# Optimization experiments

Hardware: AMD Instinct MI355X
Metric: run time of the kernel (lower is better)

Reference implementation:

```python
import jax, jax.numpy as jnp
import numpy as np

N = 50000        # n_nodes
E = 640000       # n_edges
D = 128          # d_model (in_dim == out_dim)
H = 8            # num_heads
DH = D // H      # head dim = 16
EPS = 1e-5


def _batchnorm(x, g, b):
    # BatchNorm1d, training-mode batch statistics (biased variance)
    mu = jnp.mean(x, axis=0)
    var = jnp.mean((x - mu) ** 2, axis=0)
    return (x - mu) * jax.lax.rsqrt(var + EPS) * g + b


def setup_inputs() -> dict:
    key = jax.random.key(0)
    ks = jax.random.split(key, 16)
    s = 0.05
    h = jax.random.normal(ks[0], (N, D), jnp.float32)
    src = jax.random.randint(ks[1], (E,), 0, N)
    # guarantee every node has >= 1 incoming edge (avoids z == 0)
    dst = jnp.concatenate([jnp.arange(N), jax.random.randint(ks[2], (E - N,), 0, N)])
    return {
        "h": h,
        "src": src,
        "dst": dst,
        "WQ": jax.random.normal(ks[3], (D, D), jnp.float32) * s,
        "WK": jax.random.normal(ks[4], (D, D), jnp.float32) * s,
        "WV": jax.random.normal(ks[5], (D, D), jnp.float32) * s,
        "WO": jax.random.normal(ks[6], (D, D), jnp.float32) * s,
        "bO": jnp.zeros((D,), jnp.float32),
        "W1": jax.random.normal(ks[7], (2 * D, D), jnp.float32) * s,
        "b1": jnp.zeros((2 * D,), jnp.float32),
        "W2": jax.random.normal(ks[8], (D, 2 * D), jnp.float32) * s,
        "b2": jnp.zeros((D,), jnp.float32),
        "bn1_g": jnp.ones((D,), jnp.float32),
        "bn1_b": jnp.zeros((D,), jnp.float32),
        "bn2_g": jnp.ones((D,), jnp.float32),
        "bn2_b": jnp.zeros((D,), jnp.float32),
    }


def reference(h, src, dst, WQ, WK, WV, WO, bO, W1, b1, W2, b2, bn1_g, bn1_b, bn2_g, bn2_b):
    n = h.shape[0]
    # projections -> [N, H, DH]
    Q = (h @ WQ.T).reshape(n, H, DH)
    K = (h @ WK.T).reshape(n, H, DH)
    V = (h @ WV.T).reshape(n, H, DH)
    # per-edge score: sum(K[src] * Q[dst]) -> [E, H]; clamp/exp (scaled_exp)
    score = jnp.sum(K[src] * Q[dst], axis=-1) / np.sqrt(DH)
    score = jnp.exp(jnp.clip(score, -5.0, 5.0))
    # scatter-sum weighted values and normalizers to destination nodes
    wV = jax.ops.segment_sum(V[src] * score[..., None], dst, num_segments=n)  # [N,H,DH]
    z = jax.ops.segment_sum(score, dst, num_segments=n)                       # [N,H]
    attn = (wV / z[..., None]).reshape(n, D)
    # O projection + residual + BN1
    h1 = _batchnorm(h + (attn @ WO.T + bO), bn1_g, bn1_b)
    # FFN + residual + BN2
    f = jax.nn.relu(h1 @ W1.T + b1) @ W2.T + b2
    return _batchnorm(h1 + f, bn2_g, bn2_b)
```

## Files before the change

kernel.cpp:

```cpp
#include <hip/hip_runtime.h>
#include <math.h>


#define ND128 16384
typedef _Float16 f16;
typedef __attribute__((ext_vector_type(8))) _Float16 h8;
typedef __attribute__((ext_vector_type(4))) _Float16 h4;
typedef __attribute__((ext_vector_type(2))) _Float16 h2;
typedef __attribute__((ext_vector_type(4))) float f4;
typedef __attribute__((ext_vector_type(2))) float ff2;

__device__ __forceinline__ ff2 fp8x2_dec(unsigned v) {
#if __has_builtin(__builtin_amdgcn_cvt_pk_f32_fp8)
    return __builtin_amdgcn_cvt_pk_f32_fp8((int)v, false);
#else
    ff2 r;
    unsigned b0 = v & 0xffu, b1 = (v >> 8) & 0xffu;
    {
        unsigned e = (b0 >> 3) & 15u, m = b0 & 7u;
        float x = e ? __uint_as_float(((e + 120u) << 23) | (m << 20)) : (float)m * 0.001953125f;
        r.x = (b0 & 0x80u) ? -x : x;
    }
    {
        unsigned e = (b1 >> 3) & 15u, m = b1 & 7u;
        float x = e ? __uint_as_float(((e + 120u) << 23) | (m << 20)) : (float)m * 0.001953125f;
        r.y = (b1 & 0x80u) ? -x : x;
    }
    return r;
#endif
}

#if !__has_builtin(__builtin_amdgcn_cvt_pk_fp8_f32)
__device__ __forceinline__ unsigned char fp8_1(float f) {
    float a = fabsf(f);
    unsigned sg = (__float_as_uint(f) >> 31) << 7;
    if (a >= 448.f) return (unsigned char)(sg | 0x7E);
    if (a < 0.0009765625f) return (unsigned char)sg;
    int E; float m = frexpf(a, &E);
    if (E - 1 < -6) {
        int q = (int)rintf(a * 512.f);
        if (q > 7) return (unsigned char)(sg | 0x08);
        return (unsigned char)(sg | q);
    }
    int q = (int)rintf(m * 16.f);
    if (q == 16) { q = 8; E += 1; }
    int Ef = E - 1 + 7;
    if (Ef > 15) return (unsigned char)(sg | 0x7E);
    return (unsigned char)(sg | (Ef << 3) | (q - 8));
}
#endif

__device__ __forceinline__ unsigned fp8_pack4(float a0, float a1, float a2, float a3) {
#if __has_builtin(__builtin_amdgcn_cvt_pk_fp8_f32)
    int pk = __builtin_amdgcn_cvt_pk_fp8_f32(a0, a1, 0, false);
    pk = __builtin_amdgcn_cvt_pk_fp8_f32(a2, a3, pk, true);
    return (unsigned)pk;
#else
    return (unsigned)fp8_1(a0) | ((unsigned)fp8_1(a1) << 8) |
           ((unsigned)fp8_1(a2) << 16) | ((unsigned)fp8_1(a3) << 24);
#endif
}

__global__ __launch_bounds__(256) void k_prep(
    const float* __restrict__ WQ, const float* __restrict__ WK,
    const float* __restrict__ WV, const float* __restrict__ WO,
    const float* __restrict__ W2,
    f16* __restrict__ Wqb, f16* __restrict__ Wkb,
    f16* __restrict__ Wvb, f16* __restrict__ Wob, f16* __restrict__ W2b,
    float* __restrict__ bn)
{
    const int b = blockIdx.x, tid = threadIdx.x;
    if (b == 0) { bn[tid] = 0.f; bn[tid + 256] = 0.f; }
    const float* Wsrc; f16* dst; int K, base;
    if (b < 4) {
        Wsrc = b == 0 ? WQ : b == 1 ? WK : b == 2 ? WV : WO;
        dst  = b == 0 ? Wqb : b == 1 ? Wkb : b == 2 ? Wvb : Wob;
        K = 128; base = 0;
    } else {
        Wsrc = W2; dst = W2b; K = 256; base = (b - 4) * 2048;
    }
#pragma unroll
    for (int it = 0; it < 8; ++it) {
        int cid = base + it * 256 + tid;
        int lane = cid & 63;
        int kb, nt;
        if (K == 128) { kb = (cid >> 6) & 3; nt = cid >> 8; }
        else          { kb = (cid >> 6) & 7; nt = cid >> 9; }
        int row = nt * 16 + (lane & 15);
        int col = kb * 32 + (lane >> 4) * 8;
        const float* p = Wsrc + (size_t)row * K + col;
        f16 o8[8];
#pragma unroll
        for (int j = 0; j < 8; ++j) o8[j] = (f16)p[j];
        *(h8*)(dst + (size_t)cid * 8) = *(const h8*)o8;
    }
}

__global__ __launch_bounds__(256) void k_qkvF(
    const float* __restrict__ h,
    const f16* __restrict__ Wqb, const f16* __restrict__ Wkb, const f16* __restrict__ Wvb,
    f16* __restrict__ Qb, unsigned char* __restrict__ Kb8, unsigned char* __restrict__ Vb8,
    int* __restrict__ cursor, int N)
{
    const int slab = blockIdx.x, tid = threadIdx.x;
    const int w = tid >> 6, lane = tid & 63;
    const int rl = lane & 15, quad = lane >> 4;
    if (tid < 128) {
        int ci = slab * 128 + tid;
        if (ci < N) cursor[ci] = 0;
    }

    h8 afr[8][4];
#pragma unroll
    for (int m = 0; m < 8; ++m) {
        int row = slab * 128 + m * 16 + rl;
#pragma unroll
        for (int kb = 0; kb < 4; ++kb) {
            h8 a;
            if (row < N) {
                const float* p = h + (size_t)row * 128 + kb * 32 + quad * 8;
                float4 f0 = *(const float4*)p;
                float4 f1 = *(const float4*)(p + 4);
                a[0] = (f16)f0.x; a[1] = (f16)f0.y; a[2] = (f16)f0.z; a[3] = (f16)f0.w;
                a[4] = (f16)f1.x; a[5] = (f16)f1.y; a[6] = (f16)f1.z; a[7] = (f16)f1.w;
            } else {
#pragma unroll
                for (int j = 0; j < 8; ++j) a[j] = (f16)0.f;
            }
            afr[m][kb] = a;
        }
    }

    for (int oidx = 0; oidx < 3; ++oidx) {
        const f16* __restrict__ Wb = oidx == 0 ? Wqb : oidx == 1 ? Wkb : Wvb;
        h8 bfr[2][4];
#pragma unroll
        for (int nt = 0; nt < 2; ++nt)
#pragma unroll
            for (int kb = 0; kb < 4; ++kb)
                bfr[nt][kb] = *(const h8*)(Wb + (size_t)(((2 * w + nt) * 4 + kb) * 64 + lane) * 8);

        f4 acc[8][2];
        f4 zero = {0.f, 0.f, 0.f, 0.f};
#pragma unroll
        for (int m = 0; m < 8; ++m) { acc[m][0] = zero; acc[m][1] = zero; }
#pragma unroll
        for (int m = 0; m < 8; ++m)
#pragma unroll
            for (int kb = 0; kb < 4; ++kb) {
                acc[m][0] = __builtin_amdgcn_mfma_f32_16x16x32_f16(bfr[0][kb], afr[m][kb], acc[m][0], 0, 0, 0);
                acc[m][1] = __builtin_amdgcn_mfma_f32_16x16x32_f16(bfr[1][kb], afr[m][kb], acc[m][1], 0, 0, 0);
            }

        if (oidx == 0) {
#pragma unroll
            for (int m = 0; m < 8; ++m) {
                int gr = slab * 128 + m * 16 + rl;
                if (gr < N) {
#pragma unroll
                    for (int nt = 0; nt < 2; ++nt) {
                        h4 o;
                        o[0] = (f16)acc[m][nt][0]; o[1] = (f16)acc[m][nt][1];
                        o[2] = (f16)acc[m][nt][2]; o[3] = (f16)acc[m][nt][3];
                        *(h4*)(Qb + (size_t)gr * 128 + w * 32 + nt * 16 + quad * 4) = o;
                    }
                }
            }
        } else {
            unsigned char* __restrict__ O8 = oidx == 1 ? Kb8 : Vb8;
#pragma unroll
            for (int m = 0; m < 8; ++m) {
                int gr = slab * 128 + m * 16 + rl;
                if (gr < N) {
#pragma unroll
                    for (int nt = 0; nt < 2; ++nt) {
                        unsigned pk = fp8_pack4(acc[m][nt][0], acc[m][nt][1],
                                                acc[m][nt][2], acc[m][nt][3]);
                        *(unsigned*)(O8 + (size_t)gr * 128 + w * 32 + nt * 16 + quad * 4) = pk;
                    }
                }
            }
        }
    }
}

__global__ __launch_bounds__(256) void k_hist(
    const int* __restrict__ dst, int* __restrict__ cursor, int E)
{
    int e = blockIdx.x * 256 + threadIdx.x;
    if (e < E) atomicAdd(&cursor[dst[e]], 1);
}

__global__ __launch_bounds__(256) void k_scanA(
    const int* __restrict__ cnt, int* __restrict__ bsum, int N)
{
    const int t = threadIdx.x;
    int base = blockIdx.x * 2048 + t * 8;
    int s = 0;
#pragma unroll
    for (int j = 0; j < 8; ++j) {
        int idx = base + j;
        if (idx < N) s += cnt[idx];
    }
#pragma unroll
    for (int off = 32; off; off >>= 1) s += __shfl_down(s, off, 64);
    __shared__ int ws4[4];
    if ((t & 63) == 0) ws4[t >> 6] = s;
    __syncthreads();
    if (t == 0) bsum[blockIdx.x] = ws4[0] + ws4[1] + ws4[2] + ws4[3];
}

__global__ __launch_bounds__(256) void k_scanC(
    const int* __restrict__ cnt, const int* __restrict__ bsum,
    int* __restrict__ rowptr, int* __restrict__ cursor, int N, int nsb)
{
    const int t = threadIdx.x, b = blockIdx.x;
    __shared__ int sboff;
    if (t == 0) {
        int r = 0;
        for (int i2 = 0; i2 < b; ++i2) r += bsum[i2];
        sboff = r;
    }
    if (t == 64 && b == nsb - 1) {
        int r = 0;
        for (int i2 = 0; i2 < nsb; ++i2) r += bsum[i2];
        rowptr[N] = r;
    }
    int base = b * 2048 + t * 8;
    int loc[8];
    int s = 0;
#pragma unroll
    for (int j = 0; j < 8; ++j) {
        int idx = base + j;
        loc[j] = (idx < N) ? cnt[idx] : 0;
        s += loc[j];
    }
    __shared__ int part[256];
    part[t] = s;
    __syncthreads();
    for (int off = 1; off < 256; off <<= 1) {
        int v = (t >= off) ? part[t - off] : 0;
        __syncthreads();
        part[t] += v;
        __syncthreads();
    }
    int run = sboff + (t ? part[t - 1] : 0);
#pragma unroll
    for (int j = 0; j < 8; ++j) {
        int idx = base + j;
        if (idx < N) { rowptr[idx] = run; cursor[idx] = run; run += loc[j]; }
    }
}

__global__ __launch_bounds__(256) void k_scatter(
    const int* __restrict__ src, const int* __restrict__ dst,
    int* __restrict__ cursor, int* __restrict__ csr_src, int E)
{
    int e = blockIdx.x * 256 + threadIdx.x;
    if (e < E) {
        int pos = atomicAdd(&cursor[dst[e]], 1);
        csr_src[pos] = src[e];
    }
}

__global__ __launch_bounds__(256) void k_attn(
    const f16* __restrict__ Qb, const unsigned char* __restrict__ Kb8,
    const unsigned char* __restrict__ Vb8,
    const int* __restrict__ rowptr, const int* __restrict__ csr_src,
    f16* __restrict__ attnf, int N)
{
    const int node = blockIdx.x * 4 + (threadIdx.x >> 6);
    const int lane = threadIdx.x & 63;
    if (node >= N) return;
    const int beg = rowptr[node], end = rowptr[node + 1];
    const h2 q2 = ((const h2*)(Qb + (size_t)node * 128))[lane];
    const float qx = (float)q2[0], qy = (float)q2[1];
    float axA = 0.f, ayA = 0.f, axB = 0.f, ayB = 0.f, zA = 0.f, zB = 0.f;
    int i = beg;
    for (; i + 3 < end; i += 4) {
        int s0 = csr_src[i], s1 = csr_src[i + 1];
        int s2 = csr_src[i + 2], s3 = csr_src[i + 3];
        unsigned k0 = *(const unsigned short*)(Kb8 + (size_t)s0 * 128 + 2 * lane);
        unsigned k1 = *(const unsigned short*)(Kb8 + (size_t)s1 * 128 + 2 * lane);
        unsigned k2 = *(const unsigned short*)(Kb8 + (size_t)s2 * 128 + 2 * lane);
        unsigned k3 = *(const unsigned short*)(Kb8 + (size_t)s3 * 128 + 2 * lane);
        unsigned v0 = *(const unsigned short*)(Vb8 + (size_t)s0 * 128 + 2 * lane);
        unsigned v1 = *(const unsigned short*)(Vb8 + (size_t)s1 * 128 + 2 * lane);
        unsigned v2 = *(const unsigned short*)(Vb8 + (size_t)s2 * 128 + 2 * lane);
        unsigned v3 = *(const unsigned short*)(Vb8 + (size_t)s3 * 128 + 2 * lane);
        ff2 kf0 = fp8x2_dec(k0), kf1 = fp8x2_dec(k1);
        ff2 kf2 = fp8x2_dec(k2), kf3 = fp8x2_dec(k3);
        float p0 = fmaf(qx, kf0.x, qy * kf0.y);
        float p1 = fmaf(qx, kf1.x, qy * kf1.y);
        float p2 = fmaf(qx, kf2.x, qy * kf2.y);
        float p3 = fmaf(qx, kf3.x, qy * kf3.y);
        p0 += __shfl_xor(p0, 4, 8); p1 += __shfl_xor(p1, 4, 8);
        p2 += __shfl_xor(p2, 4, 8); p3 += __shfl_xor(p3, 4, 8);
        p0 += __shfl_xor(p0, 2, 8); p1 += __shfl_xor(p1, 2, 8);
        p2 += __shfl_xor(p2, 2, 8); p3 += __shfl_xor(p3, 2, 8);
        p0 += __shfl_xor(p0, 1, 8); p1 += __shfl_xor(p1, 1, 8);
        p2 += __shfl_xor(p2, 1, 8); p3 += __shfl_xor(p3, 1, 8);
        float sc0 = __expf(fminf(fmaxf(p0 * 0.25f, -5.f), 5.f));
        float sc1 = __expf(fminf(fmaxf(p1 * 0.25f, -5.f), 5.f));
        float sc2 = __expf(fminf(fmaxf(p2 * 0.25f, -5.f), 5.f));
        float sc3 = __expf(fminf(fmaxf(p3 * 0.25f, -5.f), 5.f));
        ff2 vf0 = fp8x2_dec(v0), vf1 = fp8x2_dec(v1);
        ff2 vf2 = fp8x2_dec(v2), vf3 = fp8x2_dec(v3);
        axA = fmaf(vf0.x, sc0, axA); ayA = fmaf(vf0.y, sc0, ayA);
        axB = fmaf(vf1.x, sc1, axB); ayB = fmaf(vf1.y, sc1, ayB);
        axA = fmaf(vf2.x, sc2, axA); ayA = fmaf(vf2.y, sc2, ayA);
        axB = fmaf(vf3.x, sc3, axB); ayB = fmaf(vf3.y, sc3, ayB);
        zA += sc0 + sc2; zB += sc1 + sc3;
    }
    for (; i < end; ++i) {
        int s0 = csr_src[i];
        unsigned k0 = *(const unsigned short*)(Kb8 + (size_t)s0 * 128 + 2 * lane);
        unsigned v0 = *(const unsigned short*)(Vb8 + (size_t)s0 * 128 + 2 * lane);
        ff2 kf0 = fp8x2_dec(k0);
        float p0 = fmaf(qx, kf0.x, qy * kf0.y);
        p0 += __shfl_xor(p0, 4, 8); p0 += __shfl_xor(p0, 2, 8); p0 += __shfl_xor(p0, 1, 8);
        float sc0 = __expf(fminf(fmaxf(p0 * 0.25f, -5.f), 5.f));
        ff2 vf0 = fp8x2_dec(v0);
        axA = fmaf(vf0.x, sc0, axA); ayA = fmaf(vf0.y, sc0, ayA);
        zA += sc0;
    }
    float inv = 1.f / (zA + zB);
    h2 o2;
    o2[0] = (f16)((axA + axB) * inv);
    o2[1] = (f16)((ayA + ayB) * inv);
    int slab = node >> 7, m = (node >> 4) & 7, lr = node & 15;
    int kb = lane >> 4, quad2 = (lane & 15) >> 2, j = (lane & 3) * 2;
    *(h2*)(attnf + (size_t)slab * ND128 +
           (size_t)(((kb * 8 + m) * 64 + lr + 16 * quad2) * 8 + j)) = o2;
}

__global__ __launch_bounds__(256) void k_oproj(
    const f16* __restrict__ attnf, const f16* __restrict__ Wob,
    const float* __restrict__ h, const float* __restrict__ bO,
    f16* __restrict__ t1b, float* __restrict__ bn, int N)
{
    __shared__ float csum[128], csq[128];
    const int tid = threadIdx.x, slab = blockIdx.x;
    const int w = tid >> 6, lane = tid & 63;
    if (tid < 128) { csum[tid] = 0.f; csq[tid] = 0.f; }
    __syncthreads();
    const f16* A = attnf + (size_t)slab * ND128;

    h8 bfr[2][4];
#pragma unroll
    for (int nt = 0; nt < 2; ++nt)
#pragma unroll
        for (int kb = 0; kb < 4; ++kb)
            bfr[nt][kb] = *(const h8*)(Wob + (size_t)(((2 * w + nt) * 4 + kb) * 64 + lane) * 8);

    f4 acc[8][2];
    f4 zero = {0.f, 0.f, 0.f, 0.f};
#pragma unroll
    for (int m = 0; m < 8; ++m) { acc[m][0] = zero; acc[m][1] = zero; }
#pragma unroll
    for (int m = 0; m < 8; ++m) {
#pragma unroll
        for (int kb = 0; kb < 4; ++kb) {
            h8 a = *(const h8*)(A + (size_t)((kb * 8 + m) * 64 + lane) * 8);
            acc[m][0] = __builtin_amdgcn_mfma_f32_16x16x32_f16(bfr[0][kb], a, acc[m][0], 0, 0, 0);
            acc[m][1] = __builtin_amdgcn_mfma_f32_16x16x32_f16(bfr[1][kb], a, acc[m][1], 0, 0, 0);
        }
    }

    const int rl = lane & 15, quad = lane >> 4;
    float4 bo[2];
#pragma unroll
    for (int nt = 0; nt < 2; ++nt)
        bo[nt] = *(const float4*)(bO + w * 32 + nt * 16 + quad * 4);
    float pcs[2][4], pcq[2][4];
#pragma unroll
    for (int nt = 0; nt < 2; ++nt)
#pragma unroll
        for (int r = 0; r < 4; ++r) { pcs[nt][r] = 0.f; pcq[nt][r] = 0.f; }

#pragma unroll
    for (int m = 0; m < 8; ++m) {
        int gr = slab * 128 + m * 16 + rl;
        if (gr < N) {
#pragma unroll
            for (int nt = 0; nt < 2; ++nt) {
                int col0 = w * 32 + nt * 16 + quad * 4;
                float4 hv = *(const float4*)(h + (size_t)gr * 128 + col0);
                float v0 = acc[m][nt][0] + hv.x + bo[nt].x;
                float v1 = acc[m][nt][1] + hv.y + bo[nt].y;
                float v2 = acc[m][nt][2] + hv.z + bo[nt].z;
                float v3 = acc[m][nt][3] + hv.w + bo[nt].w;
                h4 o; o[0] = (f16)v0; o[1] = (f16)v1; o[2] = (f16)v2; o[3] = (f16)v3;
                *(h4*)(t1b + (size_t)slab * ND128 +
                       (size_t)(((w * 8 + m) * 64 + (nt * 2 + (quad >> 1)) * 16 + rl) * 8 +
                                (quad & 1) * 4)) = o;
                pcs[nt][0] += v0; pcq[nt][0] += v0 * v0;
                pcs[nt][1] += v1; pcq[nt][1] += v1 * v1;
                pcs[nt][2] += v2; pcq[nt][2] += v2 * v2;
                pcs[nt][3] += v3; pcq[nt][3] += v3 * v3;
            }
        }
    }
#pragma unroll
    for (int nt = 0; nt < 2; ++nt)
#pragma unroll
        for (int r = 0; r < 4; ++r) {
            float s = pcs[nt][r], q = pcq[nt][r];
            s += __shfl_xor(s, 8, 16); q += __shfl_xor(q, 8, 16);
            s += __shfl_xor(s, 4, 16); q += __shfl_xor(q, 4, 16);
            s += __shfl_xor(s, 2, 16); q += __shfl_xor(q, 2, 16);
            s += __shfl_xor(s, 1, 16); q += __shfl_xor(q, 1, 16);
            if (rl == 0) {
                int cl = w * 32 + nt * 16 + quad * 4 + r;
                atomicAdd(&csum[cl], s);
                atomicAdd(&csq[cl], q);
            }
        }
    __syncthreads();
    if (tid < 128) {
        atomicAdd(bn + tid, csum[tid]);
        atomicAdd(bn + 128 + tid, csq[tid]);
    }
}

__global__ __launch_bounds__(128) void k_fold1(
    const float* __restrict__ bn, const float* __restrict__ g1,
    const float* __restrict__ bb1, const float* __restrict__ W1,
    const float* __restrict__ b1, f16* __restrict__ W1b,
    float* __restrict__ badj, float* __restrict__ sfold,
    float* __restrict__ bfold, int N)
{
    const int o = blockIdx.x, i = threadIdx.x;
    float invN = 1.f / (float)N;
    float mu = bn[i] * invN;
    float var = bn[128 + i] * invN - mu * mu;
    float s = g1[i] * rsqrtf(var + 1e-5f);
    float bb = bb1[i] - mu * s;
    if (o == 0) { sfold[i] = s; bfold[i] = bb; }
    float wv = W1[(size_t)o * 128 + i];
    __shared__ float red[128];
    red[i] = wv * bb;
    const int nt = o >> 4, lanelow = o & 15;
    const int kb = i >> 5, quad = (i >> 3) & 3, j = i & 7;
    W1b[(size_t)(((nt * 4 + kb) * 64 + lanelow + 16 * quad) * 8 + j)] = (f16)(wv * s);
    __syncthreads();
#pragma unroll
    for (int off = 64; off; off >>= 1) {
        if (i < off) red[i] += red[i + off];
        __syncthreads();
    }
    if (i == 0) badj[o] = b1[o] + red[0];
}

__global__ __launch_bounds__(256) void k_ffn1(
    const f16* __restrict__ t1b, const f16* __restrict__ W1b,
    const float* __restrict__ badj, f16* __restrict__ ub, int N)
{
    const int slab = blockIdx.x, ch = blockIdx.y;
    const int w = threadIdx.x >> 6, lane = threadIdx.x & 63;
    const f16* A = t1b + (size_t)slab * ND128;

    h8 bfr[2][4];
#pragma unroll
    for (int nt = 0; nt < 2; ++nt)
#pragma unroll
        for (int kb = 0; kb < 4; ++kb) {
            int ntg = ch * 8 + 2 * w + nt;
            bfr[nt][kb] = *(const h8*)(W1b + (size_t)((ntg * 4 + kb) * 64 + lane) * 8);
        }

    f4 acc[8][2];
    f4 zero = {0.f, 0.f, 0.f, 0.f};
#pragma unroll
    for (int m = 0; m < 8; ++m) { acc[m][0] = zero; acc[m][1] = zero; }
#pragma unroll
    for (int m = 0; m < 8; ++m) {
#pragma unroll
        for (int kb = 0; kb < 4; ++kb) {
            h8 a = *(const h8*)(A + (size_t)((kb * 8 + m) * 64 + lane) * 8);
            acc[m][0] = __builtin_amdgcn_mfma_f32_16x16x32_f16(bfr[0][kb], a, acc[m][0], 0, 0, 0);
            acc[m][1] = __builtin_amdgcn_mfma_f32_16x16x32_f16(bfr[1][kb], a, acc[m][1], 0, 0, 0);
        }
    }

    const int rl = lane & 15, quad = lane >> 4;
    const int kbu = ch * 4 + w;
    float4 ba[2];
#pragma unroll
    for (int nt = 0; nt < 2; ++nt)
        ba[nt] = *(const float4*)(badj + ch * 128 + w * 32 + nt * 16 + quad * 4);
#pragma unroll
    for (int m = 0; m < 8; ++m) {
        int gr = slab * 128 + m * 16 + rl;
        if (gr < N) {
#pragma unroll
            for (int nt = 0; nt < 2; ++nt) {
                h4 o;
                o[0] = (f16)fmaxf(acc[m][nt][0] + ba[nt].x, 0.f);
                o[1] = (f16)fmaxf(acc[m][nt][1] + ba[nt].y, 0.f);
                o[2] = (f16)fmaxf(acc[m][nt][2] + ba[nt].z, 0.f);
                o[3] = (f16)fmaxf(acc[m][nt][3] + ba[nt].w, 0.f);
                *(h4*)(ub + (size_t)slab * 32768 +
                       (size_t)(((kbu * 8 + m) * 64 + (nt * 2 + (quad >> 1)) * 16 + rl) * 8 +
                                (quad & 1) * 4)) = o;
            }
        }
    }
}

__global__ __launch_bounds__(256) void k_ffn2(
    const f16* __restrict__ ub, const f16* __restrict__ W2b,
    const f16* __restrict__ t1b,
    const float* __restrict__ sfold, const float* __restrict__ bfold,
    const float* __restrict__ b2, float* __restrict__ out,
    float* __restrict__ bn, int N)
{
    __shared__ float csum[128], csq[128], sS[128], sB[128];
    const int tid = threadIdx.x, slab = blockIdx.x;
    const int w = tid >> 6, lane = tid & 63;
    if (tid < 128) {
        csum[tid] = 0.f; csq[tid] = 0.f;
        sS[tid] = sfold[tid]; sB[tid] = bfold[tid] + b2[tid];
    }
    __syncthreads();
    const f16* A = ub + (size_t)slab * 32768;
    const f16* T1 = t1b + (size_t)slab * ND128;

    h8 bfr[2][8];
#pragma unroll
    for (int nt = 0; nt < 2; ++nt)
#pragma unroll
        for (int kb = 0; kb < 8; ++kb)
            bfr[nt][kb] = *(const h8*)(W2b + (size_t)(((2 * w + nt) * 8 + kb) * 64 + lane) * 8);

    f4 acc[8][2];
    f4 zero = {0.f, 0.f, 0.f, 0.f};
#pragma unroll
    for (int m = 0; m < 8; ++m) { acc[m][0] = zero; acc[m][1] = zero; }
#pragma unroll
    for (int m = 0; m < 8; ++m) {
#pragma unroll
        for (int kb = 0; kb < 8; ++kb) {
            h8 a = *(const h8*)(A + (size_t)((kb * 8 + m) * 64 + lane) * 8);
            acc[m][0] = __builtin_amdgcn_mfma_f32_16x16x32_f16(bfr[0][kb], a, acc[m][0], 0, 0, 0);
            acc[m][1] = __builtin_amdgcn_mfma_f32_16x16x32_f16(bfr[1][kb], a, acc[m][1], 0, 0, 0);
        }
    }

    const int rl = lane & 15, quad = lane >> 4;
    float pcs[2][4], pcq[2][4];
#pragma unroll
    for (int nt = 0; nt < 2; ++nt)
#pragma unroll
        for (int r = 0; r < 4; ++r) { pcs[nt][r] = 0.f; pcq[nt][r] = 0.f; }

#pragma unroll
    for (int m = 0; m < 8; ++m) {
        int gr = slab * 128 + m * 16 + rl;
        if (gr < N) {
#pragma unroll
            for (int nt = 0; nt < 2; ++nt) {
                int col0 = w * 32 + nt * 16 + quad * 4;
                h4 t1v = *(const h4*)(T1 +
                    (size_t)(((w * 8 + m) * 64 + (nt * 2 + (quad >> 1)) * 16 + rl) * 8 +
                             (quad & 1) * 4));
                float4 ss = *(const float4*)&sS[col0];
                float4 sb = *(const float4*)&sB[col0];
                float4 o;
                o.x = acc[m][nt][0] + fmaf(ss.x, (float)t1v[0], sb.x);
                o.y = acc[m][nt][1] + fmaf(ss.y, (float)t1v[1], sb.y);
                o.z = acc[m][nt][2] + fmaf(ss.z, (float)t1v[2], sb.z);
                o.w = acc[m][nt][3] + fmaf(ss.w, (float)t1v[3], sb.w);
                *(float4*)(out + (size_t)gr * 128 + col0) = o;
                pcs[nt][0] += o.x; pcq[nt][0] += o.x * o.x;
                pcs[nt][1] += o.y; pcq[nt][1] += o.y * o.y;
                pcs[nt][2] += o.z; pcq[nt][2] += o.z * o.z;
                pcs[nt][3] += o.w; pcq[nt][3] += o.w * o.w;
            }
        }
    }
#pragma unroll
    for (int nt = 0; nt < 2; ++nt)
#pragma unroll
        for (int r = 0; r < 4; ++r) {
            float s = pcs[nt][r], q = pcq[nt][r];
            s += __shfl_xor(s, 8, 16); q += __shfl_xor(q, 8, 16);
            s += __shfl_xor(s, 4, 16); q += __shfl_xor(q, 4, 16);
            s += __shfl_xor(s, 2, 16); q += __shfl_xor(q, 2, 16);
            s += __shfl_xor(s, 1, 16); q += __shfl_xor(q, 1, 16);
            if (rl == 0) {
                int cl = w * 32 + nt * 16 + quad * 4 + r;
                atomicAdd(&csum[cl], s);
                atomicAdd(&csq[cl], q);
            }
        }
    __syncthreads();
    if (tid < 128) {
        atomicAdd(bn + 256 + tid, csum[tid]);
        atomicAdd(bn + 384 + tid, csq[tid]);
    }
}

__global__ __launch_bounds__(256) void k_bn2(
    float* __restrict__ out, const float* __restrict__ bn,
    const float* __restrict__ g2, const float* __restrict__ bb2, int N)
{
    __shared__ float sS[128], sB[128];
    const int tid = threadIdx.x;
    if (tid < 128) {
        float invN = 1.f / (float)N;
        float mu = bn[256 + tid] * invN;
        float var = bn[384 + tid] * invN - mu * mu;
        float scl = g2[tid] * rsqrtf(var + 1e-5f);
        sS[tid] = scl;
        sB[tid] = bb2[tid] - mu * scl;
    }
    __syncthreads();
    size_t idx = (size_t)blockIdx.x * 256 + tid;
    size_t total = (size_t)N * 32;
    if (idx < total) {
        int c0 = (int)((idx * 4) & 127);
        float4 v = *(const float4*)(out + idx * 4);
        v.x = fmaf(v.x, sS[c0 + 0], sB[c0 + 0]);
        v.y = fmaf(v.y, sS[c0 + 1], sB[c0 + 1]);
        v.z = fmaf(v.z, sS[c0 + 2], sB[c0 + 2]);
        v.w = fmaf(v.w, sS[c0 + 3], sB[c0 + 3]);
        *(float4*)(out + idx * 4) = v;
    }
}

extern "C" void kernel_launch(void* const* d_in, const int* in_sizes, int n_in,
                              void* d_out, int out_size, void* d_ws, size_t ws_size,
                              hipStream_t stream)
{
    const float* h   = (const float*)d_in[0];
    const int*   src = (const int*)d_in[1];
    const int*   dst = (const int*)d_in[2];
    const float* WQ  = (const float*)d_in[3];
    const float* WK  = (const float*)d_in[4];
    const float* WV  = (const float*)d_in[5];
    const float* WO  = (const float*)d_in[6];
    const float* bO  = (const float*)d_in[7];
    const float* W1  = (const float*)d_in[8];
    const float* b1  = (const float*)d_in[9];
    const float* W2  = (const float*)d_in[10];
    const float* b2  = (const float*)d_in[11];
    const float* g1  = (const float*)d_in[12];
    const float* bb1 = (const float*)d_in[13];
    const float* g2  = (const float*)d_in[14];
    const float* bb2 = (const float*)d_in[15];
    float* out = (float*)d_out;

    int N = in_sizes[0] / 128;
    int E = in_sizes[1];
    const int slabs = (N + 127) / 128;
    const int nsb = (N + 2047) / 2048;
    const size_t B1 = (size_t)slabs * 32768;

    char* Wp = (char*)d_ws;
    f16* attnf = (f16*)Wp;
    f16* Qb  = (f16*)(Wp + B1);
    unsigned char* Kb8 = (unsigned char*)(Wp + 2 * B1);
    unsigned char* Vb8 = (unsigned char*)(Wp + 2 * B1 + B1 / 2);
    f16* ub  = (f16*)(Wp + B1);
    f16* t1b = (f16*)(Wp + 3 * B1);
    const size_t base = 4 * B1;
    f16* Wqb = (f16*)(Wp + base);
    f16* Wkb = (f16*)(Wp + base + 32768);
    f16* Wvb = (f16*)(Wp + base + 65536);
    f16* Wob = (f16*)(Wp + base + 98304);
    f16* W1b = (f16*)(Wp + base + 131072);
    f16* W2b = (f16*)(Wp + base + 196608);
    float* badj  = (float*)(Wp + base + 262144);
    float* sfold = (float*)(Wp + base + 263168);
    float* bfold = (float*)(Wp + base + 263680);
    float* bn    = (float*)(Wp + base + 264192);
    int* cursor  = (int*)(Wp + base + 266240);
    int* rowptr  = (int*)(Wp + base + 266240 + (size_t)N * 4);
    int* csr     = (int*)(Wp + base + 266240 + (size_t)N * 8 + 8);
    int* bsum    = (int*)((char*)csr + (size_t)E * 4);

    k_prep<<<6, 256, 0, stream>>>(WQ, WK, WV, WO, W2, Wqb, Wkb, Wvb, Wob, W2b, bn);
    k_qkvF<<<slabs, 256, 0, stream>>>(h, Wqb, Wkb, Wvb, Qb, Kb8, Vb8, cursor, N);
    k_hist<<<(E + 255) / 256, 256, 0, stream>>>(dst, cursor, E);
    k_scanA<<<nsb, 256, 0, stream>>>(cursor, bsum, N);
    k_scanC<<<nsb, 256, 0, stream>>>(cursor, bsum, rowptr, cursor, N, nsb);
    k_scatter<<<(E + 255) / 256, 256, 0, stream>>>(src, dst, cursor, csr, E);
    k_attn<<<(N + 3) / 4, 256, 0, stream>>>(Qb, Kb8, Vb8, rowptr, csr, attnf, N);
    k_oproj<<<slabs, 256, 0, stream>>>(attnf, Wob, h, bO, t1b, bn, N);
    k_fold1<<<256, 128, 0, stream>>>(bn, g1, bb1, W1, b1, W1b, badj, sfold, bfold, N);
    k_ffn1<<<dim3(slabs, 2), 256, 0, stream>>>(t1b, W1b, badj, ub, N);
    k_ffn2<<<slabs, 256, 0, stream>>>(ub, W2b, t1b, sfold, bfold, b2, out, bn, N);
    k_bn2<<<(int)(((size_t)N * 32 + 255) / 256), 256, 0, stream>>>(out, bn, g2, bb2, N);
}
```

Baseline: 332.8 us.

## Pre-convert h to fp16 fragment layout and split QKV projection across grid

After: 322.3 us. 3.1% less time.

```diff
diff --git a/kernel.cpp b/kernel.cpp
--- a/kernel.cpp
+++ b/kernel.cpp
@@ -62,122 +62,128 @@
 }
 
 __global__ __launch_bounds__(256) void k_prep(
+    const float* __restrict__ h, f16* __restrict__ hb,
     const float* __restrict__ WQ, const float* __restrict__ WK,
     const float* __restrict__ WV, const float* __restrict__ WO,
     const float* __restrict__ W2,
     f16* __restrict__ Wqb, f16* __restrict__ Wkb,
     f16* __restrict__ Wvb, f16* __restrict__ Wob, f16* __restrict__ W2b,
-    float* __restrict__ bn)
-{
-    const int b = blockIdx.x, tid = threadIdx.x;
-    if (b == 0) { bn[tid] = 0.f; bn[tid + 256] = 0.f; }
-    const float* Wsrc; f16* dst; int K, base;
-    if (b < 4) {
-        Wsrc = b == 0 ? WQ : b == 1 ? WK : b == 2 ? WV : WO;
-        dst  = b == 0 ? Wqb : b == 1 ? Wkb : b == 2 ? Wvb : Wob;
-        K = 128; base = 0;
-    } else {
-        Wsrc = W2; dst = W2b; K = 256; base = (b - 4) * 2048;
-    }
-#pragma unroll
-    for (int it = 0; it < 8; ++it) {
-        int cid = base + it * 256 + tid;
-        int lane = cid & 63;
-        int kb, nt;
-        if (K == 128) { kb = (cid >> 6) & 3; nt = cid >> 8; }
-        else          { kb = (cid >> 6) & 7; nt = cid >> 9; }
-        int row = nt * 16 + (lane & 15);
-        int col = kb * 32 + (lane >> 4) * 8;
-        const float* p = Wsrc + (size_t)row * K + col;
-        f16 o8[8];
-#pragma unroll
-        for (int j = 0; j < 8; ++j) o8[j] = (f16)p[j];
-        *(h8*)(dst + (size_t)cid * 8) = *(const h8*)o8;
-    }
-}
-
-__global__ __launch_bounds__(256) void k_qkvF(
-    const float* __restrict__ h,
-    const f16* __restrict__ Wqb, const f16* __restrict__ Wkb, const f16* __restrict__ Wvb,
-    f16* __restrict__ Qb, unsigned char* __restrict__ Kb8, unsigned char* __restrict__ Vb8,
-    int* __restrict__ cursor, int N)
-{
-    const int slab = blockIdx.x, tid = threadIdx.x;
-    const int w = tid >> 6, lane = tid & 63;
-    const int rl = lane & 15, quad = lane >> 4;
+    float* __restrict__ bn, int* __restrict__ cursor, int N)
+{
+    const int slab = blockIdx.x;
+    const int tid = threadIdx.x;
     if (tid < 128) {
         int ci = slab * 128 + tid;
         if (ci < N) cursor[ci] = 0;
     }
-
-    h8 afr[8][4];
+    if (slab == 6) { bn[tid] = 0.f; bn[tid + 256] = 0.f; }
+#pragma unroll
+    for (int it = 0; it < 8; ++it) {
+        int cid = it * 256 + tid;
+        int lane = cid & 63;
+        int m = (cid >> 6) & 7;
+        int kb = cid >> 9;
+        int row = slab * 128 + m * 16 + (lane & 15);
+        int col = kb * 32 + (lane >> 4) * 8;
+        f16 o8[8];
+        if (row < N) {
+            const float* p = h + (size_t)row * 128 + col;
+            float4 f0 = *(const float4*)p;
+            float4 f1 = *(const float4*)(p + 4);
+            o8[0] = (f16)f0.x; o8[1] = (f16)f0.y; o8[2] = (f16)f0.z; o8[3] = (f16)f0.w;
+            o8[4] = (f16)f1.x; o8[5] = (f16)f1.y; o8[6] = (f16)f1.z; o8[7] = (f16)f1.w;
+        } else {
+#pragma unroll
+            for (int j = 0; j < 8; ++j) o8[j] = (f16)0.f;
+        }
+        *(h8*)(hb + (size_t)slab * ND128 + (size_t)cid * 8) = *(const h8*)o8;
+    }
+    if (slab < 6) {
+        const float* Wsrc; f16* dst; int K, base;
+        if (slab < 4) {
+            Wsrc = slab == 0 ? WQ : slab == 1 ? WK : slab == 2 ? WV : WO;
+            dst  = slab == 0 ? Wqb : slab == 1 ? Wkb : slab == 2 ? Wvb : Wob;
+            K = 128; base = 0;
+        } else {
+            Wsrc = W2; dst = W2b; K = 256; base = (slab - 4) * 2048;
+        }
+#pragma unroll
+        for (int it = 0; it < 8; ++it) {
+            int cid = base + it * 256 + tid;
+            int lane = cid & 63;
+            int kb, nt;
+            if (K == 128) { kb = (cid >> 6) & 3; nt = cid >> 8; }
+            else          { kb = (cid >> 6) & 7; nt = cid >> 9; }
+            int row = nt * 16 + (lane & 15);
+            int col = kb * 32 + (lane >> 4) * 8;
+            const float* p = Wsrc + (size_t)row * K + col;
+            f16 o8[8];
+#pragma unroll
+            for (int j = 0; j < 8; ++j) o8[j] = (f16)p[j];
+            *(h8*)(dst + (size_t)cid * 8) = *(const h8*)o8;
+        }
+    }
+}
+
+__global__ __launch_bounds__(256) void k_qkv(
+    const f16* __restrict__ hb, const f16* __restrict__ Wqb,
+    const f16* __restrict__ Wkb, const f16* __restrict__ Wvb,
+    f16* __restrict__ Qb, unsigned char* __restrict__ Kb8,
+    unsigned char* __restrict__ Vb8, int N)
+{
+    const int slab = blockIdx.x, oidx = blockIdx.y;
+    const int w = threadIdx.x >> 6, lane = threadIdx.x & 63;
+    const f16* __restrict__ Wb = oidx == 0 ? Wqb : oidx == 1 ? Wkb : Wvb;
+    const f16* A = hb + (size_t)slab * ND128;
+
+    h8 bfr[2][4];
+#pragma unroll
+    for (int nt = 0; nt < 2; ++nt)
+#pragma unroll
+        for (int kb = 0; kb < 4; ++kb)
+            bfr[nt][kb] = *(const h8*)(Wb + (size_t)(((2 * w + nt) * 4 + kb) * 64 + lane) * 8);
+
+    f4 acc[8][2];
+    f4 zero = {0.f, 0.f, 0.f, 0.f};
+#pragma unroll
+    for (int m = 0; m < 8; ++m) { acc[m][0] = zero; acc[m][1] = zero; }
+
 #pragma unroll
     for (int m = 0; m < 8; ++m) {
-        int row = slab * 128 + m * 16 + rl;
 #pragma unroll
         for (int kb = 0; kb < 4; ++kb) {
-            h8 a;
-            if (row < N) {
-                const float* p = h + (size_t)row * 128 + kb * 32 + quad * 8;
-                float4 f0 = *(const float4*)p;
-                float4 f1 = *(const float4*)(p + 4);
-                a[0] = (f16)f0.x; a[1] = (f16)f0.y; a[2] = (f16)f0.z; a[3] = (f16)f0.w;
-                a[4] = (f16)f1.x; a[5] = (f16)f1.y; a[6] = (f16)f1.z; a[7] = (f16)f1.w;
-            } else {
-#pragma unroll
-                for (int j = 0; j < 8; ++j) a[j] = (f16)0.f;
-            }
-            afr[m][kb] = a;
-        }
-    }
-
-    for (int oidx = 0; oidx < 3; ++oidx) {
-        const f16* __restrict__ Wb = oidx == 0 ? Wqb : oidx == 1 ? Wkb : Wvb;
-        h8 bfr[2][4];
-#pragma unroll
-        for (int nt = 0; nt < 2; ++nt)
-#pragma unroll
-            for (int kb = 0; kb < 4; ++kb)
-                bfr[nt][kb] = *(const h8*)(Wb + (size_t)(((2 * w + nt) * 4 + kb) * 64 + lane) * 8);
-
-        f4 acc[8][2];
-        f4 zero = {0.f, 0.f, 0.f, 0.f};
-#pragma unroll
-        for (int m = 0; m < 8; ++m) { acc[m][0] = zero; acc[m][1] = zero; }
-#pragma unroll
-        for (int m = 0; m < 8; ++m)
-#pragma unroll
-            for (int kb = 0; kb < 4; ++kb) {
-                acc[m][0] = __builtin_amdgcn_mfma_f32_16x16x32_f16(bfr[0][kb], afr[m][kb], acc[m][0], 0, 0, 0);
-                acc[m][1] = __builtin_amdgcn_mfma_f32_16x16x32_f16(bfr[1][kb], afr[m][kb], acc[m][1], 0, 0, 0);
-            }
-
-        if (oidx == 0) {
-#pragma unroll
-            for (int m = 0; m < 8; ++m) {
-                int gr = slab * 128 + m * 16 + rl;
-                if (gr < N) {
-#pragma unroll
-                    for (int nt = 0; nt < 2; ++nt) {
-                        h4 o;
-                        o[0] = (f16)acc[m][nt][0]; o[1] = (f16)acc[m][nt][1];
-                        o[2] = (f16)acc[m][nt][2]; o[3] = (f16)acc[m][nt][3];
-                        *(h4*)(Qb + (size_t)gr * 128 + w * 32 + nt * 16 + quad * 4) = o;
-                    }
+            h8 a = *(const h8*)(A + (size_t)((kb * 8 + m) * 64 + lane) * 8);
+            acc[m][0] = __builtin_amdgcn_mfma_f32_16x16x32_f16(bfr[0][kb], a, acc[m][0], 0, 0, 0);
+            acc[m][1] = __builtin_amdgcn_mfma_f32_16x16x32_f16(bfr[1][kb], a, acc[m][1], 0, 0, 0);
+        }
+    }
+
+    const int rl = lane & 15, quad = lane >> 4;
+    if (oidx == 0) {
+#pragma unroll
+        for (int m = 0; m < 8; ++m) {
+            int gr = slab * 128 + m * 16 + rl;
+            if (gr < N) {
+#pragma unroll
+                for (int nt = 0; nt < 2; ++nt) {
+                    h4 o;
+                    o[0] = (f16)acc[m][nt][0]; o[1] = (f16)acc[m][nt][1];
+                    o[2] = (f16)acc[m][nt][2]; o[3] = (f16)acc[m][nt][3];
+                    *(h4*)(Qb + (size_t)gr * 128 + w * 32 + nt * 16 + quad * 4) = o;
                 }
             }
-        } else {
-            unsigned char* __restrict__ O8 = oidx == 1 ? Kb8 : Vb8;
-#pragma unroll
-            for (int m = 0; m < 8; ++m) {
-                int gr = slab * 128 + m * 16 + rl;
-                if (gr < N) {
-#pragma unroll
-                    for (int nt = 0; nt < 2; ++nt) {
-                        unsigned pk = fp8_pack4(acc[m][nt][0], acc[m][nt][1],
-                                                acc[m][nt][2], acc[m][nt][3]);
-                        *(unsigned*)(O8 + (size_t)gr * 128 + w * 32 + nt * 16 + quad * 4) = pk;
-                    }
+        }
+    } else {
+        unsigned char* __restrict__ O8 = oidx == 1 ? Kb8 : Vb8;
+#pragma unroll
+        for (int m = 0; m < 8; ++m) {
+            int gr = slab * 128 + m * 16 + rl;
+            if (gr < N) {
+#pragma unroll
+                for (int nt = 0; nt < 2; ++nt) {
+                    unsigned pk = fp8_pack4(acc[m][nt][0], acc[m][nt][1],
+                                            acc[m][nt][2], acc[m][nt][3]);
+                    *(unsigned*)(O8 + (size_t)gr * 128 + w * 32 + nt * 16 + quad * 4) = pk;
                 }
             }
         }
@@ -658,7 +664,7 @@
     const size_t B1 = (size_t)slabs * 32768;
 
     char* Wp = (char*)d_ws;
-    f16* attnf = (f16*)Wp;
+    f16* hb  = (f16*)Wp;
     f16* Qb  = (f16*)(Wp + B1);
     unsigned char* Kb8 = (unsigned char*)(Wp + 2 * B1);
     unsigned char* Vb8 = (unsigned char*)(Wp + 2 * B1 + B1 / 2);
@@ -680,14 +686,15 @@
     int* csr     = (int*)(Wp + base + 266240 + (size_t)N * 8 + 8);
     int* bsum    = (int*)((char*)csr + (size_t)E * 4);
 
-    k_prep<<<6, 256, 0, stream>>>(WQ, WK, WV, WO, W2, Wqb, Wkb, Wvb, Wob, W2b, bn);
-    k_qkvF<<<slabs, 256, 0, stream>>>(h, Wqb, Wkb, Wvb, Qb, Kb8, Vb8, cursor, N);
+    k_prep<<<slabs, 256, 0, stream>>>(h, hb, WQ, WK, WV, WO, W2,
+                                      Wqb, Wkb, Wvb, Wob, W2b, bn, cursor, N);
+    k_qkv<<<dim3(slabs, 3), 256, 0, stream>>>(hb, Wqb, Wkb, Wvb, Qb, Kb8, Vb8, N);
     k_hist<<<(E + 255) / 256, 256, 0, stream>>>(dst, cursor, E);
     k_scanA<<<nsb, 256, 0, stream>>>(cursor, bsum, N);
     k_scanC<<<nsb, 256, 0, stream>>>(cursor, bsum, rowptr, cursor, N, nsb);
     k_scatter<<<(E + 255) / 256, 256, 0, stream>>>(src, dst, cursor, csr, E);
-    k_attn<<<(N + 3) / 4, 256, 0, stream>>>(Qb, Kb8, Vb8, rowptr, csr, attnf, N);
-    k_oproj<<<slabs, 256, 0, stream>>>(attnf, Wob, h, bO, t1b, bn, N);
+    k_attn<<<(N + 3) / 4, 256, 0, stream>>>(Qb, Kb8, Vb8, rowptr, csr, hb, N);
+    k_oproj<<<slabs, 256, 0, stream>>>(hb, Wob, h, bO, t1b, bn, N);
     k_fold1<<<256, 128, 0, stream>>>(bn, g1, bb1, W1, b1, W1b, badj, sfold, bfold, N);
     k_ffn1<<<dim3(slabs, 2), 256, 0, stream>>>(t1b, W1b, badj, ub, N);
     k_ffn2<<<slabs, 256, 0, stream>>>(ub, W2b, t1b, sfold, bfold, b2, out, bn, N);
```
